# Kernel optimization log

Measured on AMD Instinct MI355X. Metric: run time of the kernel, lower is better.

The kernel has to match this reference:

```python
import jax, jax.numpy as jnp
import numpy as np

NR = 100000   # router nodes
NP = 200000   # packet nodes
H = 128       # h_dim
E_PASS = 600000   # router -> router
E_CONN = 600000   # packet -> router
E_TRANS = 600000  # router -> packet


def setup_inputs() -> dict:
    key = jax.random.key(0)
    ks = jax.random.split(key, 12)
    return {
        "router_feat": jax.random.normal(ks[0], (NR, H), jnp.float32),
        "packet_feat": jax.random.normal(ks[1], (NP, H), jnp.float32),
        "W_r": jax.random.normal(ks[2], (2 * H, H), jnp.float32) * 0.05,
        "b_r": jax.random.normal(ks[3], (H,), jnp.float32) * 0.05,
        "W_p": jax.random.normal(ks[4], (H, H), jnp.float32) * 0.05,
        "b_p": jax.random.normal(ks[5], (H,), jnp.float32) * 0.05,
        "pass_src": jax.random.randint(ks[6], (E_PASS,), 0, NR, jnp.int32),
        "pass_dst": jax.random.randint(ks[7], (E_PASS,), 0, NR, jnp.int32),
        "connect_src": jax.random.randint(ks[8], (E_CONN,), 0, NP, jnp.int32),
        "connect_dst": jax.random.randint(ks[9], (E_CONN,), 0, NR, jnp.int32),
        "transfer_src": jax.random.randint(ks[10], (E_TRANS,), 0, NR, jnp.int32),
        "transfer_dst": jax.random.randint(ks[11], (E_TRANS,), 0, NP, jnp.int32),
    }


def reference(router_feat, packet_feat, W_r, b_r, W_p, b_p,
              pass_src, pass_dst, connect_src, connect_dst,
              transfer_src, transfer_dst):
    # relation 'pass': router -> router, copy_u + sum -> h1 (router)
    h1_r = jax.ops.segment_sum(router_feat[pass_src], pass_dst, num_segments=NR)
    # relation 'connect': packet -> router, copy_u + sum -> h2 (router)
    h2_r = jax.ops.segment_sum(packet_feat[connect_src], connect_dst, num_segments=NR)
    # relation 'transfer': router -> packet, copy_u + mean -> h1 (packet)
    s = jax.ops.segment_sum(router_feat[transfer_src], transfer_dst, num_segments=NP)
    cnt = jax.ops.segment_sum(jnp.ones((E_TRANS,), jnp.float32), transfer_dst,
                              num_segments=NP)
    # DGL mean: zero for zero in-degree nodes
    h1_p = s / jnp.maximum(cnt, 1.0)[:, None]

    # router update: feat += ReLU(Linear(concat([h1, h2])))
    router_out = router_feat + jax.nn.relu(
        jnp.concatenate([h1_r, h2_r], axis=-1) @ W_r + b_r)
    # packet update: feat += ReLU(Linear(h1))
    packet_out = packet_feat + jax.nn.relu(h1_p @ W_p + b_p)
    return router_out, packet_out
```

## Files before the change

kernel.cpp:

```cpp
#include <hip/hip_runtime.h>

#define H_DIM 128

typedef __attribute__((ext_vector_type(8))) short short8v;
typedef __attribute__((ext_vector_type(4))) float f32x4;

__device__ __forceinline__ ushort f2bf(float f) {
  unsigned u = __builtin_bit_cast(unsigned, f);
  u += 0x7fffu + ((u >> 16) & 1u);
  return (ushort)(u >> 16);
}
__device__ __forceinline__ float bflo(unsigned u) {
  return __builtin_bit_cast(float, u << 16);
}
__device__ __forceinline__ float bfhi(unsigned u) {
  return __builtin_bit_cast(float, u & 0xffff0000u);
}
__device__ __forceinline__ short8v pack_bf8(float4 a0, float4 a1) {
  short8v af;
  af[0] = (short)f2bf(a0.x);
  af[1] = (short)f2bf(a0.y);
  af[2] = (short)f2bf(a0.z);
  af[3] = (short)f2bf(a0.w);
  af[4] = (short)f2bf(a1.x);
  af[5] = (short)f2bf(a1.y);
  af[6] = (short)f2bf(a1.z);
  af[7] = (short)f2bf(a1.w);
  return af;
}

__global__ __launch_bounds__(256) void histcast_k(
    const float* __restrict__ W_r, const float* __restrict__ W_p,
    ushort* __restrict__ Wt, const int* __restrict__ d0,
    const int* __restrict__ d1, const int* __restrict__ d2,
    int* __restrict__ ro, int* __restrict__ rank, int n0, int n1, int n2,
    int NRn) {
  int bid = blockIdx.x;
  if (bid < 192) {
    int i = bid * 256 + threadIdx.x;
    int m = i >> 14;
    int j = (i >> 7) & 127;
    int k = i & 127;
    float v = (m == 0)   ? W_r[k * 128 + j]
              : (m == 1) ? W_r[(128 + k) * 128 + j]
                         : W_p[k * 128 + j];
    Wt[i] = f2bf(v);
  } else {
    int e = (bid - 192) * 256 + threadIdx.x;
    int slot;
    if (e < n0)
      slot = d0[e];
    else if (e < n0 + n1)
      slot = NRn + d1[e - n0];
    else if (e < n0 + n1 + n2)
      slot = 2 * NRn + d2[e - n0 - n1];
    else
      return;
    rank[e] = atomicAdd(&ro[slot], 1);
  }
}

__global__ __launch_bounds__(256) void scan1_k(int* __restrict__ a, int n,
                                               int* __restrict__ bsums) {
  __shared__ int ts[256];
  int t = threadIdx.x;
  int base = blockIdx.x * 2048 + t * 8;
  int v[8];
  int s = 0;
#pragma unroll
  for (int k = 0; k < 8; ++k) {
    v[k] = (base + k < n) ? a[base + k] : 0;
    s += v[k];
  }
  ts[t] = s;
  __syncthreads();
  for (int off = 1; off < 256; off <<= 1) {
    int x = (t >= off) ? ts[t - off] : 0;
    __syncthreads();
    ts[t] += x;
    __syncthreads();
  }
  if (t == 0) bsums[blockIdx.x] = ts[255];
  int run = (t == 0) ? 0 : ts[t - 1];
#pragma unroll
  for (int k = 0; k < 8; ++k) {
    int x = v[k];
    if (base + k < n) a[base + k] = run;
    run += x;
  }
}

__global__ __launch_bounds__(256) void scan23_k(int* __restrict__ a, int n,
                                                const int* __restrict__ bsums,
                                                int nb, int total) {
  __shared__ int ts[256];
  int t = threadIdx.x;
  int v = (t < nb) ? bsums[t] : 0;
  ts[t] = v;
  __syncthreads();
  for (int off = 1; off < 256; off <<= 1) {
    int x = (t >= off) ? ts[t - off] : 0;
    __syncthreads();
    ts[t] += x;
    __syncthreads();
  }
  int b = blockIdx.x;
  int excl = (b == 0) ? 0 : ts[b - 1];
  int base = b * 2048;
#pragma unroll
  for (int k = 0; k < 8; ++k) {
    int i = base + k * 256 + t;
    if (i < n) a[i] += excl;
  }
  if (b == 0 && t == 0) a[n] = total;
}

__global__ __launch_bounds__(256) void permgemm_k(
    const float* __restrict__ rf, const float* __restrict__ pf,
    const ushort* __restrict__ Wt, ushort* __restrict__ Y1,
    ushort* __restrict__ Y2, ushort* __restrict__ Yp,
    const int* __restrict__ s0a, const int* __restrict__ d0a,
    const int* __restrict__ s1a, const int* __restrict__ d1a,
    const int* __restrict__ s2a, const int* __restrict__ d2a,
    const int* __restrict__ ro, const int* __restrict__ rank,
    int* __restrict__ es, int nb1, int nb2, int M1, int M2, int n0, int n1,
    int n2, int NRn, int ng, int np) {
  __shared__ float lds_f[8192];
  long T = (long)ng + np;
  long b = blockIdx.x;
  int g_before = (int)((b * ng) / T);
  int g_incl = (int)(((b + 1) * ng) / T);
  bool do_gemm = g_incl > g_before;
  int idx = do_gemm ? g_before : (int)(b - g_before);

  if (!do_gemm) {
    long e = (long)idx * 256 + threadIdx.x;
    int src, slot;
    if (e < n0) {
      slot = d0a[e];
      src = s0a[e];
    } else if (e < n0 + n1) {
      long i = e - n0;
      slot = NRn + d1a[i];
      src = s1a[i];
    } else if (e < n0 + n1 + n2) {
      long i = e - n0 - n1;
      slot = 2 * NRn + d2a[i];
      src = s2a[i];
    } else
      return;
    es[ro[slot] + rank[e]] = src;
    return;
  }

  ushort* wl = (ushort*)lds_f;
  const float* X;
  ushort* Y;
  const ushort* Wg;
  int M, row0;
  if (idx < nb1) {
    X = rf; Y = Y1; Wg = Wt; M = M1; row0 = idx * 128;
  } else if (idx < nb1 + nb2) {
    X = pf; Y = Y2; Wg = Wt + 16384; M = M2; row0 = (idx - nb1) * 128;
  } else {
    X = rf; Y = Yp; Wg = Wt + 32768; M = M1; row0 = (idx - nb1 - nb2) * 128;
  }

  int tid = threadIdx.x;
  {
    const uint4* src = (const uint4*)Wg;
    for (int i = tid; i < 2048; i += 256) {
      int j = i >> 4;
      int k8 = (i & 15) * 8;
      int kk = k8 ^ ((j & 7) << 3);
      *(uint4*)&wl[j * 128 + kk] = src[i];
    }
  }
  __syncthreads();

  int lane = tid & 63;
  int wv = tid >> 6;
  int l15 = lane & 15;
  int kq = lane >> 4;
  int rowl = wv * 16 + l15;
  int g0 = row0 + rowl;
  int g1 = row0 + 64 + rowl;
  int gc0 = g0 < M ? g0 : M - 1;
  int gc1 = g1 < M ? g1 : M - 1;

  f32x4 acc0[8], acc1[8];
#pragma unroll
  for (int t = 0; t < 8; ++t) {
    f32x4 z = {0.f, 0.f, 0.f, 0.f};
    acc0[t] = z;
    acc1[t] = z;
  }

#pragma unroll
  for (int ks = 0; ks < 4; ++ks) {
    int k0 = ks * 32;
    const float* ap0 = X + (long)gc0 * H_DIM + k0 + kq * 8;
    const float* ap1 = X + (long)gc1 * H_DIM + k0 + kq * 8;
    float4 a00 = *(const float4*)ap0;
    float4 a01 = *(const float4*)(ap0 + 4);
    float4 a10 = *(const float4*)ap1;
    float4 a11 = *(const float4*)(ap1 + 4);
    short8v af0 = pack_bf8(a00, a01);
    short8v af1 = pack_bf8(a10, a11);
#pragma unroll
    for (int nt = 0; nt < 8; ++nt) {
      int j = nt * 16 + l15;
      int kk = (k0 + kq * 8) ^ ((j & 7) << 3);
      short8v bf = *(const short8v*)&wl[j * 128 + kk];
      acc0[nt] =
          __builtin_amdgcn_mfma_f32_16x16x32_bf16(af0, bf, acc0[nt], 0, 0, 0);
      acc1[nt] =
          __builtin_amdgcn_mfma_f32_16x16x32_bf16(af1, bf, acc1[nt], 0, 0, 0);
    }
  }

  __syncthreads();
#pragma unroll
  for (int nt = 0; nt < 8; ++nt) {
#pragma unroll
    for (int r = 0; r < 4; ++r) {
      int rl = wv * 16 + kq * 4 + r;
      int col = (nt * 16 + l15) ^ (kq << 4);
      lds_f[rl * 128 + col] = acc0[nt][r];
    }
  }
  __syncthreads();
  for (int i = tid; i < 2048; i += 256) {
    int flat = i * 4;
    int r = flat >> 7;
    int cc = flat & 127;
    int sw = ((r >> 2) & 3) << 4;
    int gr = row0 + r;
    if (gr < M) {
      float4 v = *(const float4*)&lds_f[r * 128 + (cc ^ sw)];
      ushort4 o;
      o.x = f2bf(v.x);
      o.y = f2bf(v.y);
      o.z = f2bf(v.z);
      o.w = f2bf(v.w);
      *(ushort4*)&Y[(long)gr * H_DIM + cc] = o;
    }
  }
  __syncthreads();
#pragma unroll
  for (int nt = 0; nt < 8; ++nt) {
#pragma unroll
    for (int r = 0; r < 4; ++r) {
      int rl = wv * 16 + kq * 4 + r;
      int col = (nt * 16 + l15) ^ (kq << 4);
      lds_f[rl * 128 + col] = acc1[nt][r];
    }
  }
  __syncthreads();
  for (int i = tid; i < 2048; i += 256) {
    int flat = i * 4;
    int r = flat >> 7;
    int cc = flat & 127;
    int sw = ((r >> 2) & 3) << 4;
    int gr = row0 + 64 + r;
    if (gr < M) {
      float4 v = *(const float4*)&lds_f[r * 128 + (cc ^ sw)];
      ushort4 o;
      o.x = f2bf(v.x);
      o.y = f2bf(v.y);
      o.z = f2bf(v.z);
      o.w = f2bf(v.w);
      *(ushort4*)&Y[(long)gr * H_DIM + cc] = o;
    }
  }
}

__device__ __forceinline__ void gacc16(const ushort* __restrict__ Y,
                                       const int* __restrict__ es, int e0,
                                       int e1, int c8, float* a) {
  int e = e0;
  for (; e + 3 < e1; e += 4) {
    uint4 v0 = *(const uint4*)(Y + (long)es[e] * H_DIM + c8);
    uint4 v1 = *(const uint4*)(Y + (long)es[e + 1] * H_DIM + c8);
    uint4 v2 = *(const uint4*)(Y + (long)es[e + 2] * H_DIM + c8);
    uint4 v3 = *(const uint4*)(Y + (long)es[e + 3] * H_DIM + c8);
    a[0] += (bflo(v0.x) + bflo(v1.x)) + (bflo(v2.x) + bflo(v3.x));
    a[1] += (bfhi(v0.x) + bfhi(v1.x)) + (bfhi(v2.x) + bfhi(v3.x));
    a[2] += (bflo(v0.y) + bflo(v1.y)) + (bflo(v2.y) + bflo(v3.y));
    a[3] += (bfhi(v0.y) + bfhi(v1.y)) + (bfhi(v2.y) + bfhi(v3.y));
    a[4] += (bflo(v0.z) + bflo(v1.z)) + (bflo(v2.z) + bflo(v3.z));
    a[5] += (bfhi(v0.z) + bfhi(v1.z)) + (bfhi(v2.z) + bfhi(v3.z));
    a[6] += (bflo(v0.w) + bflo(v1.w)) + (bflo(v2.w) + bflo(v3.w));
    a[7] += (bfhi(v0.w) + bfhi(v1.w)) + (bfhi(v2.w) + bfhi(v3.w));
  }
  for (; e < e1; ++e) {
    uint4 v = *(const uint4*)(Y + (long)es[e] * H_DIM + c8);
    a[0] += bflo(v.x);
    a[1] += bfhi(v.x);
    a[2] += bflo(v.y);
    a[3] += bfhi(v.y);
    a[4] += bflo(v.z);
    a[5] += bfhi(v.z);
    a[6] += bflo(v.w);
    a[7] += bfhi(v.w);
  }
}

__global__ __launch_bounds__(256) void gather_k(
    const ushort* __restrict__ Y1, const ushort* __restrict__ Y2,
    const ushort* __restrict__ Yp, const int* __restrict__ ro,
    const int* __restrict__ es, const float* __restrict__ rf,
    const float* __restrict__ pf, const float* __restrict__ b_r,
    const float* __restrict__ b_p, float* __restrict__ out_r,
    float* __restrict__ out_p, int nrb, int NRn, int NPn) {
  int tid = threadIdx.x;
  int lane = tid & 63;
  int wv = tid >> 6;
  int sub = lane >> 4;
  int c8 = (lane & 15) * 8;
  int bid = blockIdx.x;

  if (bid < nrb) {
    int row = bid * 16 + wv * 4 + sub;
    if (row >= NRn) return;
    const f32x4* rp = (const f32x4*)&rf[(long)row * H_DIM + c8];
    f32x4 rv0 = __builtin_nontemporal_load(rp);
    f32x4 rv1 = __builtin_nontemporal_load(rp + 1);
    float4 bb0 = *(const float4*)&b_r[c8];
    float4 bb1 = *(const float4*)&b_r[c8 + 4];
    float a[8] = {0.f, 0.f, 0.f, 0.f, 0.f, 0.f, 0.f, 0.f};
    float c[8] = {0.f, 0.f, 0.f, 0.f, 0.f, 0.f, 0.f, 0.f};
    gacc16(Y1, es, ro[row], ro[row + 1], c8, a);
    gacc16(Y2, es, ro[NRn + row], ro[NRn + row + 1], c8, c);
    float bv[8] = {bb0.x, bb0.y, bb0.z, bb0.w, bb1.x, bb1.y, bb1.z, bb1.w};
    f32x4 o0, o1;
#pragma unroll
    for (int i = 0; i < 4; ++i) {
      float v = (a[i] + c[i]) + bv[i];
      v = v > 0.f ? v : 0.f;
      o0[i] = rv0[i] + v;
      float v2 = (a[i + 4] + c[i + 4]) + bv[i + 4];
      v2 = v2 > 0.f ? v2 : 0.f;
      o1[i] = rv1[i] + v2;
    }
    f32x4* op = (f32x4*)&out_r[(long)row * H_DIM + c8];
    __builtin_nontemporal_store(o0, op);
    __builtin_nontemporal_store(o1, op + 1);
  } else {
    int row = (bid - nrb) * 16 + wv * 4 + sub;
    if (row >= NPn) return;
    const f32x4* pp = (const f32x4*)&pf[(long)row * H_DIM + c8];
    f32x4 pv0 = __builtin_nontemporal_load(pp);
    f32x4 pv1 = __builtin_nontemporal_load(pp + 1);
    float4 bb0 = *(const float4*)&b_p[c8];
    float4 bb1 = *(const float4*)&b_p[c8 + 4];
    int e0 = ro[2 * NRn + row], e1 = ro[2 * NRn + row + 1];
    float a[8] = {0.f, 0.f, 0.f, 0.f, 0.f, 0.f, 0.f, 0.f};
    gacc16(Yp, es, e0, e1, c8, a);
    int deg = e1 - e0;
    float inv = 1.0f / (float)(deg > 1 ? deg : 1);
    float bv[8] = {bb0.x, bb0.y, bb0.z, bb0.w, bb1.x, bb1.y, bb1.z, bb1.w};
    f32x4 o0, o1;
#pragma unroll
    for (int i = 0; i < 4; ++i) {
      float v = a[i] * inv + bv[i];
      v = v > 0.f ? v : 0.f;
      o0[i] = pv0[i] + v;
      float v2 = a[i + 4] * inv + bv[i + 4];
      v2 = v2 > 0.f ? v2 : 0.f;
      o1[i] = pv1[i] + v2;
    }
    f32x4* op = (f32x4*)&out_p[(long)row * H_DIM + c8];
    __builtin_nontemporal_store(o0, op);
    __builtin_nontemporal_store(o1, op + 1);
  }
}

extern "C" void kernel_launch(void* const* d_in, const int* in_sizes, int n_in,
                              void* d_out, int out_size, void* d_ws,
                              size_t ws_size, hipStream_t stream) {
  const float* router_feat = (const float*)d_in[0];
  const float* packet_feat = (const float*)d_in[1];
  const float* W_r = (const float*)d_in[2];
  const float* b_r = (const float*)d_in[3];
  const float* W_p = (const float*)d_in[4];
  const float* b_p = (const float*)d_in[5];
  const int* pass_src = (const int*)d_in[6];
  const int* pass_dst = (const int*)d_in[7];
  const int* connect_src = (const int*)d_in[8];
  const int* connect_dst = (const int*)d_in[9];
  const int* transfer_src = (const int*)d_in[10];
  const int* transfer_dst = (const int*)d_in[11];

  const int NRn = in_sizes[0] / H_DIM;
  const int NPn = in_sizes[1] / H_DIM;
  const int E0 = in_sizes[6], E1 = in_sizes[8], E2 = in_sizes[10];
  const long Etot = (long)E0 + E1 + E2;
  const int nseg = 2 * NRn + NPn;

  float* out_r = (float*)d_out;
  float* out_p = out_r + (size_t)NRn * H_DIM;

  int* ro = (int*)d_ws;
  int* rank = ro + (nseg + 1);
  int* es = rank + Etot;
  int* bsums = es + Etot;
  size_t int_count = (size_t)(nseg + 1) + 2 * (size_t)Etot + 256;
  size_t byte_off = ((int_count * 4) + 15) & ~(size_t)15;
  ushort* Y1 = (ushort*)((char*)d_ws + byte_off);
  ushort* Y2 = Y1 + (size_t)NRn * H_DIM;
  ushort* Yp = Y2 + (size_t)NPn * H_DIM;
  ushort* Wt = Yp + (size_t)NRn * H_DIM;

  (void)hipMemsetAsync(ro, 0, (size_t)(nseg + 1) * sizeof(int), stream);

  int egrid = (int)((Etot + 255) / 256);
  histcast_k<<<192 + egrid, 256, 0, stream>>>(W_r, W_p, Wt, pass_dst,
                                              connect_dst, transfer_dst, ro,
                                              rank, E0, E1, E2, NRn);
  int nb = (nseg + 2047) / 2048;
  scan1_k<<<nb, 256, 0, stream>>>(ro, nseg, bsums);
  scan23_k<<<nb, 256, 0, stream>>>(ro, nseg, bsums, nb, (int)Etot);

  int nb1 = (NRn + 127) / 128, nb2 = (NPn + 127) / 128, nb3 = nb1;
  int ng = nb1 + nb2 + nb3;
  int np = egrid;
  permgemm_k<<<ng + np, 256, 0, stream>>>(
      router_feat, packet_feat, Wt, Y1, Y2, Yp, pass_src, pass_dst, connect_src,
      connect_dst, transfer_src, transfer_dst, ro, rank, es, nb1, nb2, NRn, NPn,
      E0, E1, E2, NRn, ng, np);

  int nrb = (NRn + 15) / 16, npb = (NPn + 15) / 16;
  gather_k<<<nrb + npb, 256, 0, stream>>>(Y1, Y2, Yp, ro, es, router_feat,
                                          packet_feat, b_r, b_p, out_r, out_p,
                                          nrb, NRn, NPn);
}
```

Measured before the change: 319.9 us.

## Fold block-offset scan into last-block pass and interleave router gathers

Drops the separate scan-add kernel. The last block to finish scan1 now scans the block sums into a small bscan table, and consumers add bscan[slot>>11] to the per-block local offsets when they read them. This removes one launch and a full read-modify-write pass over the offsets array, at the cost of an extra lookup per offset read. The router gather also interleaves the pass and connect edge loops two at a time to keep more independent loads in flight.

Measured after the change: 339.6 us. 6.2% more time.

```diff
diff --git a/kernel.cpp b/kernel.cpp
--- a/kernel.cpp
+++ b/kernel.cpp
@@ -61,8 +61,11 @@
 }
 
 __global__ __launch_bounds__(256) void scan1_k(int* __restrict__ a, int n,
-                                               int* __restrict__ bsums) {
+                                               int* __restrict__ bsums,
+                                               int* __restrict__ bscan,
+                                               int* __restrict__ cnt, int nb) {
   __shared__ int ts[256];
+  __shared__ bool amlast;
   int t = threadIdx.x;
   int base = blockIdx.x * 2048 + t * 8;
   int v[8];
@@ -88,31 +91,26 @@
     if (base + k < n) a[base + k] = run;
     run += x;
   }
-}
-
-__global__ __launch_bounds__(256) void scan23_k(int* __restrict__ a, int n,
-                                                const int* __restrict__ bsums,
-                                                int nb, int total) {
-  __shared__ int ts[256];
-  int t = threadIdx.x;
-  int v = (t < nb) ? bsums[t] : 0;
-  ts[t] = v;
-  __syncthreads();
-  for (int off = 1; off < 256; off <<= 1) {
-    int x = (t >= off) ? ts[t - off] : 0;
+  __threadfence();
+  __syncthreads();
+  if (t == 0) {
+    int old = atomicAdd(cnt, 1);
+    amlast = (old == gridDim.x - 1);
+  }
+  __syncthreads();
+  if (amlast) {
+    __threadfence();
+    int bv = (t < nb) ? bsums[t] : 0;
+    ts[t] = bv;
     __syncthreads();
-    ts[t] += x;
-    __syncthreads();
-  }
-  int b = blockIdx.x;
-  int excl = (b == 0) ? 0 : ts[b - 1];
-  int base = b * 2048;
-#pragma unroll
-  for (int k = 0; k < 8; ++k) {
-    int i = base + k * 256 + t;
-    if (i < n) a[i] += excl;
-  }
-  if (b == 0 && t == 0) a[n] = total;
+    for (int off = 1; off < 256; off <<= 1) {
+      int x = (t >= off) ? ts[t - off] : 0;
+      __syncthreads();
+      ts[t] += x;
+      __syncthreads();
+    }
+    if (t < nb) bscan[t] = (t == 0) ? 0 : ts[t - 1];
+  }
 }
 
 __global__ __launch_bounds__(256) void permgemm_k(
@@ -122,9 +120,9 @@
     const int* __restrict__ s0a, const int* __restrict__ d0a,
     const int* __restrict__ s1a, const int* __restrict__ d1a,
     const int* __restrict__ s2a, const int* __restrict__ d2a,
-    const int* __restrict__ ro, const int* __restrict__ rank,
-    int* __restrict__ es, int nb1, int nb2, int M1, int M2, int n0, int n1,
-    int n2, int NRn, int ng, int np) {
+    const int* __restrict__ ro, const int* __restrict__ bscan,
+    const int* __restrict__ rank, int* __restrict__ es, int nb1, int nb2,
+    int M1, int M2, int n0, int n1, int n2, int NRn, int ng, int np) {
   __shared__ float lds_f[8192];
   long T = (long)ng + np;
   long b = blockIdx.x;
@@ -149,7 +147,7 @@
       src = s2a[i];
     } else
       return;
-    es[ro[slot] + rank[e]] = src;
+    es[ro[slot] + bscan[slot >> 11] + rank[e]] = src;
     return;
   }
 
@@ -309,10 +307,11 @@
 __global__ __launch_bounds__(256) void gather_k(
     const ushort* __restrict__ Y1, const ushort* __restrict__ Y2,
     const ushort* __restrict__ Yp, const int* __restrict__ ro,
-    const int* __restrict__ es, const float* __restrict__ rf,
-    const float* __restrict__ pf, const float* __restrict__ b_r,
-    const float* __restrict__ b_p, float* __restrict__ out_r,
-    float* __restrict__ out_p, int nrb, int NRn, int NPn) {
+    const int* __restrict__ bscan, const int* __restrict__ es,
+    const float* __restrict__ rf, const float* __restrict__ pf,
+    const float* __restrict__ b_r, const float* __restrict__ b_p,
+    float* __restrict__ out_r, float* __restrict__ out_p, int nrb, int NRn,
+    int NPn, int nseg, int Etot) {
   int tid = threadIdx.x;
   int lane = tid & 63;
   int wv = tid >> 6;
@@ -328,10 +327,37 @@
     f32x4 rv1 = __builtin_nontemporal_load(rp + 1);
     float4 bb0 = *(const float4*)&b_r[c8];
     float4 bb1 = *(const float4*)&b_r[c8 + 4];
+    int sA = ro[row] + bscan[row >> 11];
+    int eA = ro[row + 1] + bscan[(row + 1) >> 11];
+    int sB = ro[NRn + row] + bscan[(NRn + row) >> 11];
+    int eB = ro[NRn + row + 1] + bscan[(NRn + row + 1) >> 11];
     float a[8] = {0.f, 0.f, 0.f, 0.f, 0.f, 0.f, 0.f, 0.f};
     float c[8] = {0.f, 0.f, 0.f, 0.f, 0.f, 0.f, 0.f, 0.f};
-    gacc16(Y1, es, ro[row], ro[row + 1], c8, a);
-    gacc16(Y2, es, ro[NRn + row], ro[NRn + row + 1], c8, c);
+    int ea = sA, eb = sB;
+    for (; ea + 1 < eA && eb + 1 < eB; ea += 2, eb += 2) {
+      uint4 va0 = *(const uint4*)(Y1 + (long)es[ea] * H_DIM + c8);
+      uint4 va1 = *(const uint4*)(Y1 + (long)es[ea + 1] * H_DIM + c8);
+      uint4 vb0 = *(const uint4*)(Y2 + (long)es[eb] * H_DIM + c8);
+      uint4 vb1 = *(const uint4*)(Y2 + (long)es[eb + 1] * H_DIM + c8);
+      a[0] += bflo(va0.x) + bflo(va1.x);
+      a[1] += bfhi(va0.x) + bfhi(va1.x);
+      a[2] += bflo(va0.y) + bflo(va1.y);
+      a[3] += bfhi(va0.y) + bfhi(va1.y);
+      a[4] += bflo(va0.z) + bflo(va1.z);
+      a[5] += bfhi(va0.z) + bfhi(va1.z);
+      a[6] += bflo(va0.w) + bflo(va1.w);
+      a[7] += bfhi(va0.w) + bfhi(va1.w);
+      c[0] += bflo(vb0.x) + bflo(vb1.x);
+      c[1] += bfhi(vb0.x) + bfhi(vb1.x);
+      c[2] += bflo(vb0.y) + bflo(vb1.y);
+      c[3] += bfhi(vb0.y) + bfhi(vb1.y);
+      c[4] += bflo(vb0.z) + bflo(vb1.z);
+      c[5] += bfhi(vb0.z) + bfhi(vb1.z);
+      c[6] += bflo(vb0.w) + bflo(vb1.w);
+      c[7] += bfhi(vb0.w) + bfhi(vb1.w);
+    }
+    gacc16(Y1, es, ea, eA, c8, a);
+    gacc16(Y2, es, eb, eB, c8, c);
     float bv[8] = {bb0.x, bb0.y, bb0.z, bb0.w, bb1.x, bb1.y, bb1.z, bb1.w};
     f32x4 o0, o1;
 #pragma unroll
@@ -354,7 +380,10 @@
     f32x4 pv1 = __builtin_nontemporal_load(pp + 1);
     float4 bb0 = *(const float4*)&b_p[c8];
     float4 bb1 = *(const float4*)&b_p[c8 + 4];
-    int e0 = ro[2 * NRn + row], e1 = ro[2 * NRn + row + 1];
+    int s = 2 * NRn + row;
+    int e0 = ro[s] + bscan[s >> 11];
+    int e1 =
+        (s + 1 == nseg) ? Etot : ro[s + 1] + bscan[(s + 1) >> 11];
     float a[8] = {0.f, 0.f, 0.f, 0.f, 0.f, 0.f, 0.f, 0.f};
     gacc16(Yp, es, e0, e1, c8, a);
     int deg = e1 - e0;
@@ -402,36 +431,37 @@
   float* out_p = out_r + (size_t)NRn * H_DIM;
 
   int* ro = (int*)d_ws;
-  int* rank = ro + (nseg + 1);
+  int* cnt = ro + (nseg + 1);
+  int* bsums = cnt + 1;
+  int* bscan = bsums + 256;
+  int* rank = bscan + 256;
   int* es = rank + Etot;
-  int* bsums = es + Etot;
-  size_t int_count = (size_t)(nseg + 1) + 2 * (size_t)Etot + 256;
+  size_t int_count = (size_t)(nseg + 1) + 1 + 512 + 2 * (size_t)Etot;
   size_t byte_off = ((int_count * 4) + 15) & ~(size_t)15;
   ushort* Y1 = (ushort*)((char*)d_ws + byte_off);
   ushort* Y2 = Y1 + (size_t)NRn * H_DIM;
   ushort* Yp = Y2 + (size_t)NPn * H_DIM;
   ushort* Wt = Yp + (size_t)NRn * H_DIM;
 
-  (void)hipMemsetAsync(ro, 0, (size_t)(nseg + 1) * sizeof(int), stream);
+  (void)hipMemsetAsync(ro, 0, (size_t)(nseg + 2) * sizeof(int), stream);
 
   int egrid = (int)((Etot + 255) / 256);
   histcast_k<<<192 + egrid, 256, 0, stream>>>(W_r, W_p, Wt, pass_dst,
                                               connect_dst, transfer_dst, ro,
                                               rank, E0, E1, E2, NRn);
   int nb = (nseg + 2047) / 2048;
-  scan1_k<<<nb, 256, 0, stream>>>(ro, nseg, bsums);
-  scan23_k<<<nb, 256, 0, stream>>>(ro, nseg, bsums, nb, (int)Etot);
+  scan1_k<<<nb, 256, 0, stream>>>(ro, nseg, bsums, bscan, cnt, nb);
 
   int nb1 = (NRn + 127) / 128, nb2 = (NPn + 127) / 128, nb3 = nb1;
   int ng = nb1 + nb2 + nb3;
   int np = egrid;
   permgemm_k<<<ng + np, 256, 0, stream>>>(
       router_feat, packet_feat, Wt, Y1, Y2, Yp, pass_src, pass_dst, connect_src,
-      connect_dst, transfer_src, transfer_dst, ro, rank, es, nb1, nb2, NRn, NPn,
-      E0, E1, E2, NRn, ng, np);
+      connect_dst, transfer_src, transfer_dst, ro, bscan, rank, es, nb1, nb2,
+      NRn, NPn, E0, E1, E2, NRn, ng, np);
 
   int nrb = (NRn + 15) / 16, npb = (NPn + 15) / 16;
-  gather_k<<<nrb + npb, 256, 0, stream>>>(Y1, Y2, Yp, ro, es, router_feat,
-                                          packet_feat, b_r, b_p, out_r, out_p,
-                                          nrb, NRn, NPn);
-}
+  gather_k<<<nrb + npb, 256, 0, stream>>>(
+      Y1, Y2, Yp, ro, bscan, es, router_feat, packet_feat, b_r, b_p, out_r,
+      out_p, nrb, NRn, NPn, nseg, (int)Etot);
+}
```
